# Optimization experiments

Measured on AMD Instinct MI355X. Metric: run time of the kernel, lower is better.

## Reference

```python
import jax, jax.numpy as jnp
import numpy as np

NHID = 512
T_K, T_Q, B = 256, 128, 8


def setup_inputs() -> dict:
    key = jax.random.key(0)
    k1, k2, k3, k4, k5 = jax.random.split(key, 5)
    query = jax.random.normal(k1, (T_Q, B, NHID), dtype=jnp.float32)
    c_key = jax.random.normal(k2, (T_K, B, NHID), dtype=jnp.float32)
    mask = jax.random.randint(k3, (T_K, B), 0, 2).astype(bool)
    # att_mlp params: Linear(2*nhid, nhid) -> Tanh -> Linear(nhid, 1)
    # stored as [in, out] so y = x @ W + b (torch Linear weight transposed)
    W1 = jax.random.normal(k4, (2 * NHID, NHID), dtype=jnp.float32) / np.sqrt(2 * NHID)
    b1 = jnp.zeros((NHID,), dtype=jnp.float32)
    W2 = jax.random.normal(k5, (NHID, 1), dtype=jnp.float32) / np.sqrt(NHID)
    b2 = jnp.zeros((1,), dtype=jnp.float32)
    return {"query": query, "c_key": c_key, "mask": mask,
            "W1": W1, "b1": b1, "W2": W2, "b2": b2}


def reference(query, c_key, mask, W1, b1, W2, b2):
    H = query.shape[-1]
    # cat([k_expand, q_expand], -1) @ W1 == k @ W1[:H] + q @ W1[H:]
    # (avoids materializing the [T_k, T_q, B, 2H] concat the torch code builds)
    k_proj = jnp.einsum('kbh,hd->kbd', c_key, W1[:H])   # [T_k, B, H]
    q_proj = jnp.einsum('qbh,hd->qbd', query, W1[H:])   # [T_q, B, H]
    h = jnp.tanh(k_proj[:, None, :, :] + q_proj[None, :, :, :] + b1)  # [T_k, T_q, B, H]
    att_score = jnp.einsum('kqbh,ho->kqb', h, W2) + b2[0]             # [T_k, T_q, B]
    att_score = jnp.where(mask[:, None, :], -jnp.inf, att_score)
    att_prob = jax.nn.softmax(att_score, axis=0)                      # softmax over keys
    # c_val defaults to c_key in the original forward
    ant_vec = jnp.einsum('kqb,kbh->qbh', att_prob, c_key)             # [T_q, B, H]
    return ant_vec, att_prob
```

## Files before the change

### kernel.cpp

```cpp
#include <hip/hip_runtime.h>
#include <math.h>

#define NHID 512
#define T_K  256
#define T_Q  128
#define BB   8

constexpr float C2L2E = 2.8853900817779268f;
constexpr float L2E   = 1.4426950408889634f;

__device__ __forceinline__ float fexp2(float x) { return __builtin_amdgcn_exp2f(x); }
__device__ __forceinline__ float frcp(float x)  { return __builtin_amdgcn_rcpf(x); }

typedef __attribute__((ext_vector_type(8))) short bf16x8;
typedef __attribute__((ext_vector_type(4))) float f32x4;

__device__ __forceinline__ unsigned short f2bf(float x) {
    unsigned u = __builtin_bit_cast(unsigned, x);
    unsigned r = (u + 0x7FFFu + ((u >> 16) & 1u)) >> 16;
    return (unsigned short)r;
}
__device__ __forceinline__ float bf2f(unsigned short h) {
    unsigned u = ((unsigned)h) << 16;
    return __builtin_bit_cast(float, u);
}

__global__ __launch_bounds__(256) void convert_w1_kernel(
    const float* __restrict__ W1,
    unsigned short* __restrict__ bt_hi, unsigned short* __restrict__ bt_lo)
{
    const int tb = blockIdx.x;
    const int kt = tb & 15;
    const int nt = tb >> 4;
    __shared__ float tile[64][65];
    const int t  = threadIdx.x;
    const int r  = t >> 2;
    const int c0 = (t & 3) * 16;
    const float* src = W1 + (size_t)(kt * 64 + r) * 512 + nt * 64 + c0;
    #pragma unroll
    for (int j = 0; j < 4; ++j) {
        const float4 v = *(const float4*)&src[j * 4];
        tile[r][c0 + j * 4 + 0] = v.x; tile[r][c0 + j * 4 + 1] = v.y;
        tile[r][c0 + j * 4 + 2] = v.z; tile[r][c0 + j * 4 + 3] = v.w;
    }
    __syncthreads();
    const size_t dst = (size_t)((kt >> 3) * 512 + nt * 64 + r) * 512
                     + (size_t)((kt & 7) * 64 + c0);
    #pragma unroll
    for (int j4 = 0; j4 < 4; ++j4) {
        ushort4 h, l;
        #pragma unroll
        for (int e = 0; e < 4; ++e) {
            const float x = tile[c0 + j4 * 4 + e][r];
            const unsigned short hb = f2bf(x);
            ((unsigned short*)&h)[e] = hb;
            ((unsigned short*)&l)[e] = f2bf(x - bf2f(hb));
        }
        *(ushort4*)&bt_hi[dst + j4 * 4] = h;
        *(ushort4*)&bt_lo[dst + j4 * 4] = l;
    }
}

__global__ __launch_bounds__(256) void proj_kernel(
    const float* __restrict__ qry, const float* __restrict__ ckey,
    const unsigned short* __restrict__ bt_hi, const unsigned short* __restrict__ bt_lo,
    const float* __restrict__ b1,
    float* __restrict__ ek, float* __restrict__ eq)
{
    const int row0 = blockIdx.x * 64;
    const int col0 = blockIdx.y * 64;
    const bool isK = row0 < 2048;
    const int bhalf = isK ? 0 : 512;

    __shared__ __align__(16) unsigned short As_h[64 * 64];
    __shared__ __align__(16) unsigned short As_l[64 * 64];
    __shared__ __align__(16) unsigned short Bs_h[64 * 64];
    __shared__ __align__(16) unsigned short Bs_l[64 * 64];

    const int t    = threadIdx.x;
    const int wave = t >> 6;
    const int lane = t & 63;
    const int wm = (wave & 1) * 32;
    const int wn = (wave >> 1) * 32;

    f32x4 acc[2][2] = {};

    const int sr = t >> 2;
    const int sc = (t & 3) * 16;
    const float* gA = (isK ? ckey + (size_t)(row0 + sr) * 512
                           : qry  + (size_t)(row0 - 2048 + sr) * 512) + sc;
    const unsigned short* gBh = bt_hi + (size_t)(bhalf + col0 + sr) * 512 + sc;
    const unsigned short* gBl = bt_lo + (size_t)(bhalf + col0 + sr) * 512 + sc;
    const int c0c = sc >> 3;
    const int sw0 = ((c0c + 0) ^ (sr & 7)) * 8;
    const int sw1 = ((c0c + 1) ^ (sr & 7)) * 8;

    const int quad = lane >> 4, fr = lane & 15;

    for (int k0 = 0; k0 < 512; k0 += 64) {
        __syncthreads();
        {
            float fa[16];
            *(float4*)&fa[0]  = *(const float4*)&gA[k0 + 0];
            *(float4*)&fa[4]  = *(const float4*)&gA[k0 + 4];
            *(float4*)&fa[8]  = *(const float4*)&gA[k0 + 8];
            *(float4*)&fa[12] = *(const float4*)&gA[k0 + 12];
            union { uint4 v; unsigned short s[8]; } h0, l0, h1, l1;
            #pragma unroll
            for (int e = 0; e < 8; ++e) {
                const unsigned short hb = f2bf(fa[e]);
                h0.s[e] = hb; l0.s[e] = f2bf(fa[e] - bf2f(hb));
            }
            #pragma unroll
            for (int e = 0; e < 8; ++e) {
                const unsigned short hb = f2bf(fa[8 + e]);
                h1.s[e] = hb; l1.s[e] = f2bf(fa[8 + e] - bf2f(hb));
            }
            *(uint4*)&As_h[sr * 64 + sw0] = h0.v; *(uint4*)&As_h[sr * 64 + sw1] = h1.v;
            *(uint4*)&As_l[sr * 64 + sw0] = l0.v; *(uint4*)&As_l[sr * 64 + sw1] = l1.v;
            uint4 v0, v1;
            v0 = *(const uint4*)&gBh[k0];     v1 = *(const uint4*)&gBh[k0 + 8];
            *(uint4*)&Bs_h[sr * 64 + sw0] = v0; *(uint4*)&Bs_h[sr * 64 + sw1] = v1;
            v0 = *(const uint4*)&gBl[k0];     v1 = *(const uint4*)&gBl[k0 + 8];
            *(uint4*)&Bs_l[sr * 64 + sw0] = v0; *(uint4*)&Bs_l[sr * 64 + sw1] = v1;
        }
        __syncthreads();
        #pragma unroll
        for (int ks = 0; ks < 2; ++ks) {
            const int cchunk = ks * 4 + quad;
            bf16x8 afh[2], afl[2], bfh[2], bfl[2];
            #pragma unroll
            for (int mt = 0; mt < 2; ++mt) {
                const int m = wm + mt * 16 + fr;
                afh[mt] = *(const bf16x8*)&As_h[m * 64 + ((cchunk ^ (m & 7)) * 8)];
                afl[mt] = *(const bf16x8*)&As_l[m * 64 + ((cchunk ^ (m & 7)) * 8)];
            }
            #pragma unroll
            for (int nt = 0; nt < 2; ++nt) {
                const int n = wn + nt * 16 + fr;
                bfh[nt] = *(const bf16x8*)&Bs_h[n * 64 + ((cchunk ^ (n & 7)) * 8)];
                bfl[nt] = *(const bf16x8*)&Bs_l[n * 64 + ((cchunk ^ (n & 7)) * 8)];
            }
            #pragma unroll
            for (int mt = 0; mt < 2; ++mt)
                #pragma unroll
                for (int nt = 0; nt < 2; ++nt) {
                    acc[mt][nt] = __builtin_amdgcn_mfma_f32_16x16x32_bf16(afh[mt], bfh[nt], acc[mt][nt], 0, 0, 0);
                    acc[mt][nt] = __builtin_amdgcn_mfma_f32_16x16x32_bf16(afh[mt], bfl[nt], acc[mt][nt], 0, 0, 0);
                    acc[mt][nt] = __builtin_amdgcn_mfma_f32_16x16x32_bf16(afl[mt], bfh[nt], acc[mt][nt], 0, 0, 0);
                }
        }
    }

    #pragma unroll
    for (int nt = 0; nt < 2; ++nt) {
        const int colg = col0 + wn + nt * 16 + fr;
        const float b1v = b1[colg];
        #pragma unroll
        for (int mt = 0; mt < 2; ++mt) {
            #pragma unroll
            for (int i = 0; i < 4; ++i) {
                const int rowg = row0 + wm + mt * 16 + quad * 4 + i;
                const float v = acc[mt][nt][i];
                if (isK) ek[(size_t)rowg * 512 + colg] = fexp2((v + b1v) * C2L2E);
                else     eq[(size_t)(rowg - 2048) * 512 + colg] = fexp2(v * C2L2E);
            }
        }
    }
}

__global__ __launch_bounds__(256) void scoreav_kernel(
    const float* __restrict__ ek, const float* __restrict__ eq,
    const float* __restrict__ W2, const float* __restrict__ b2,
    const int* __restrict__ mask, const float* __restrict__ ckey,
    float* __restrict__ prob_out, float* __restrict__ out_ant)
{
    const int t    = threadIdx.x;
    const int lane = t & 63;
    const int wave = __builtin_amdgcn_readfirstlane(t >> 6);
    const int q0   = blockIdx.x * 2;
    const int b    = blockIdx.y;
    const int myk  = wave * 64 + lane;

    __shared__ float eks[2][256 * 19];
    __shared__ float ps[2][256];
    __shared__ float pacc[4][2][512];

    const float4 wA = *(const float4*)&W2[lane * 4];
    const float4 wB = *(const float4*)&W2[256 + lane * 4];
    float s2 = wA.x + wA.y + wA.z + wA.w + wB.x + wB.y + wB.z + wB.w;
    #pragma unroll
    for (int m = 32; m; m >>= 1) s2 += __shfl_xor(s2, m, 64);
    const float base = s2 + b2[0];

    const float* __restrict__ eqr0 = eq + (size_t)(q0 * 8 + b) * 512;
    const float* __restrict__ eqr1 = eq + (size_t)((q0 + 1) * 8 + b) * 512;

    const float* __restrict__ ekg = ek + ((size_t)t * 8 + b) * 512;

    {
        float fa[16];
        *(float4*)&fa[0]  = *(const float4*)&ekg[0];
        *(float4*)&fa[4]  = *(const float4*)&ekg[4];
        *(float4*)&fa[8]  = *(const float4*)&ekg[8];
        *(float4*)&fa[12] = *(const float4*)&ekg[12];
        #pragma unroll
        for (int j = 0; j < 16; ++j) eks[0][t * 19 + j] = fa[j];
    }
    __syncthreads();

    float racc0 = 0.0f, racc1 = 0.0f;

    for (int chunk = 0; chunk < 32; ++chunk) {
        const int buf = chunk & 1;
        const int hc  = chunk * 16;
        float nf[16];
        if (chunk < 31) {
            *(float4*)&nf[0]  = *(const float4*)&ekg[hc + 16];
            *(float4*)&nf[4]  = *(const float4*)&ekg[hc + 20];
            *(float4*)&nf[8]  = *(const float4*)&ekg[hc + 24];
            *(float4*)&nf[12] = *(const float4*)&ekg[hc + 28];
        }
        #pragma unroll
        for (int s = 0; s < 8; ++s) {
            const float ek0 = eks[buf][myk * 19 + 2 * s + 0];
            const float ek1 = eks[buf][myk * 19 + 2 * s + 1];
            const int h = hc + 2 * s;
            const float w0 = W2[h], w1 = W2[h + 1];
            const float e0 = eqr0[h], e1 = eqr0[h + 1];
            const float f0 = eqr1[h], f1 = eqr1[h + 1];
            {
                const float t0 = ek0 * e0, t1 = ek1 * e1;
                const float a0 = t0 + 1.0f, a1 = t1 + 1.0f;
                const float den = a0 * a1;
                const float num = fmaf(w0, a1, w1 * a0);
                racc0 = fmaf(num, frcp(den), racc0);
            }
            {
                const float t0 = ek0 * f0, t1 = ek1 * f1;
                const float a0 = t0 + 1.0f, a1 = t1 + 1.0f;
                const float den = a0 * a1;
                const float num = fmaf(w0, a1, w1 * a0);
                racc1 = fmaf(num, frcp(den), racc1);
            }
        }
        __syncthreads();
        if (chunk < 31) {
            const int nb = buf ^ 1;
            #pragma unroll
            for (int j = 0; j < 16; ++j) eks[nb][t * 19 + j] = nf[j];
        }
        __syncthreads();
    }

    {
        const int msk = mask[myk * 8 + b];
        float s0 = base - 2.0f * racc0;
        float s1 = base - 2.0f * racc1;
        if (msk) { s0 = -INFINITY; s1 = -INFINITY; }
        ps[0][myk] = s0;
        ps[1][myk] = s1;
    }
    __syncthreads();

    if (wave < 2) {
        float4 sv = *(const float4*)&ps[wave][lane * 4];
        float m = fmaxf(fmaxf(sv.x, sv.y), fmaxf(sv.z, sv.w));
        #pragma unroll
        for (int d = 32; d; d >>= 1) m = fmaxf(m, __shfl_xor(m, d, 64));
        float4 pv;
        pv.x = fexp2((sv.x - m) * L2E);
        pv.y = fexp2((sv.y - m) * L2E);
        pv.z = fexp2((sv.z - m) * L2E);
        pv.w = fexp2((sv.w - m) * L2E);
        float sum = pv.x + pv.y + pv.z + pv.w;
        #pragma unroll
        for (int d = 32; d; d >>= 1) sum += __shfl_xor(sum, d, 64);
        const float inv = frcp(sum);
        pv.x *= inv; pv.y *= inv; pv.z *= inv; pv.w *= inv;
        *(float4*)&ps[wave][lane * 4] = pv;
        const int qb_idx = (q0 + wave) * 8 + b;
        const int kbase = lane * 4;
        prob_out[(size_t)(kbase + 0) * 1024 + qb_idx] = pv.x;
        prob_out[(size_t)(kbase + 1) * 1024 + qb_idx] = pv.y;
        prob_out[(size_t)(kbase + 2) * 1024 + qb_idx] = pv.z;
        prob_out[(size_t)(kbase + 3) * 1024 + qb_idx] = pv.w;
    }
    __syncthreads();

    {
        const int h0 = lane * 8;
        float4 aL0 = {}, aH0 = {}, aL1 = {}, aH1 = {};
        const int kstart = wave * 64;
        #pragma unroll 4
        for (int ki = 0; ki < 64; ++ki) {
            const int k = kstart + ki;
            const float* ckp = &ckey[((size_t)k * 8 + b) * 512 + h0];
            const float4 c0 = *(const float4*)&ckp[0];
            const float4 c1 = *(const float4*)&ckp[4];
            const float p0 = ps[0][k];
            const float p1 = ps[1][k];
            aL0.x = fmaf(p0, c0.x, aL0.x); aL0.y = fmaf(p0, c0.y, aL0.y);
            aL0.z = fmaf(p0, c0.z, aL0.z); aL0.w = fmaf(p0, c0.w, aL0.w);
            aH0.x = fmaf(p0, c1.x, aH0.x); aH0.y = fmaf(p0, c1.y, aH0.y);
            aH0.z = fmaf(p0, c1.z, aH0.z); aH0.w = fmaf(p0, c1.w, aH0.w);
            aL1.x = fmaf(p1, c0.x, aL1.x); aL1.y = fmaf(p1, c0.y, aL1.y);
            aL1.z = fmaf(p1, c0.z, aL1.z); aL1.w = fmaf(p1, c0.w, aL1.w);
            aH1.x = fmaf(p1, c1.x, aH1.x); aH1.y = fmaf(p1, c1.y, aH1.y);
            aH1.z = fmaf(p1, c1.z, aH1.z); aH1.w = fmaf(p1, c1.w, aH1.w);
        }
        *(float4*)&pacc[wave][0][h0 + 0] = aL0;
        *(float4*)&pacc[wave][0][h0 + 4] = aH0;
        *(float4*)&pacc[wave][1][h0 + 0] = aL1;
        *(float4*)&pacc[wave][1][h0 + 4] = aH1;
    }
    __syncthreads();

    {
        const int h2 = t * 2;
        #pragma unroll
        for (int qi = 0; qi < 2; ++qi) {
            float2 r0 = *(const float2*)&pacc[0][qi][h2];
            float2 r1 = *(const float2*)&pacc[1][qi][h2];
            float2 r2 = *(const float2*)&pacc[2][qi][h2];
            float2 r3 = *(const float2*)&pacc[3][qi][h2];
            float2 r;
            r.x = (r0.x + r1.x) + (r2.x + r3.x);
            r.y = (r0.y + r1.y) + (r2.y + r3.y);
            *(float2*)&out_ant[((size_t)(q0 + qi) * 8 + b) * 512 + h2] = r;
        }
    }
}

extern "C" void kernel_launch(void* const* d_in, const int* in_sizes, int n_in,
                              void* d_out, int out_size, void* d_ws, size_t ws_size,
                              hipStream_t stream)
{
    const float* qry  = (const float*)d_in[0];
    const float* ckey = (const float*)d_in[1];
    const int*   mask = (const int*)d_in[2];
    const float* W1   = (const float*)d_in[3];
    const float* b1   = (const float*)d_in[4];
    const float* W2   = (const float*)d_in[5];
    const float* b2   = (const float*)d_in[6];

    float* out_ant  = (float*)d_out;
    float* out_prob = (float*)d_out + T_Q * BB * NHID;

    float* ws = (float*)d_ws;
    float* ws_ek = ws;
    float* ws_eq = ws + 1048576;
    unsigned short* bt_hi = (unsigned short*)(ws + 1572864);
    unsigned short* bt_lo = (unsigned short*)(ws + 1835008);

    convert_w1_kernel<<<dim3(128), 256, 0, stream>>>(W1, bt_hi, bt_lo);
    proj_kernel<<<dim3(48, 8), 256, 0, stream>>>(qry, ckey, bt_hi, bt_lo, b1, ws_ek, ws_eq);
    scoreav_kernel<<<dim3(64, 8), 256, 0, stream>>>(ws_ek, ws_eq, W2, b2, mask, ckey,
                                                    out_prob, out_ant);
}
```

Baseline: 126.3 us.

## Transpose exp(k_proj) to [b][h][k] and stream it directly in score kernel

The projection kernel now writes the key-side exponentials in a transposed [batch][hidden][key] layout, so each score thread reads coalesced global loads for its key without LDS staging. The query rows and W2 are staged once into shared memory, which replaces the per-chunk double-buffered LDS tile and its two barriers per chunk. The projection kernel's stores become strided (stride 256 floats along the key index), which may cost write efficiency. The score loop then relies on L2/global latency hiding through unrolling.

After: 118.6 us. 6.1% less time.

```diff
diff --git a/kernel.cpp b/kernel.cpp
--- a/kernel.cpp
+++ b/kernel.cpp
@@ -65,7 +65,7 @@
     const float* __restrict__ qry, const float* __restrict__ ckey,
     const unsigned short* __restrict__ bt_hi, const unsigned short* __restrict__ bt_lo,
     const float* __restrict__ b1,
-    float* __restrict__ ek, float* __restrict__ eq)
+    float* __restrict__ ekt, float* __restrict__ eq)
 {
     const int row0 = blockIdx.x * 64;
     const int col0 = blockIdx.y * 64;
@@ -162,15 +162,20 @@
             for (int i = 0; i < 4; ++i) {
                 const int rowg = row0 + wm + mt * 16 + quad * 4 + i;
                 const float v = acc[mt][nt][i];
-                if (isK) ek[(size_t)rowg * 512 + colg] = fexp2((v + b1v) * C2L2E);
-                else     eq[(size_t)(rowg - 2048) * 512 + colg] = fexp2(v * C2L2E);
+                if (isK) {
+                    const int kidx = rowg >> 3;
+                    const int bb   = rowg & 7;
+                    ekt[((size_t)bb * 512 + colg) * 256 + kidx] = fexp2((v + b1v) * C2L2E);
+                } else {
+                    eq[(size_t)(rowg - 2048) * 512 + colg] = fexp2(v * C2L2E);
+                }
             }
         }
     }
 }
 
 __global__ __launch_bounds__(256) void scoreav_kernel(
-    const float* __restrict__ ek, const float* __restrict__ eq,
+    const float* __restrict__ ekt, const float* __restrict__ eq,
     const float* __restrict__ W2, const float* __restrict__ b2,
     const int* __restrict__ mask, const float* __restrict__ ckey,
     float* __restrict__ prob_out, float* __restrict__ out_ant)
@@ -180,11 +185,19 @@
     const int wave = __builtin_amdgcn_readfirstlane(t >> 6);
     const int q0   = blockIdx.x * 2;
     const int b    = blockIdx.y;
-    const int myk  = wave * 64 + lane;
-
-    __shared__ float eks[2][256 * 19];
+
+    __shared__ float eq0s[512], eq1s[512], w2s[512];
     __shared__ float ps[2][256];
     __shared__ float pacc[4][2][512];
+
+    {
+        const float2 v0 = *(const float2*)&eq[((size_t)q0 * 8 + b) * 512 + t * 2];
+        const float2 v1 = *(const float2*)&eq[((size_t)(q0 + 1) * 8 + b) * 512 + t * 2];
+        const float2 w  = *(const float2*)&W2[t * 2];
+        *(float2*)&eq0s[t * 2] = v0;
+        *(float2*)&eq1s[t * 2] = v1;
+        *(float2*)&w2s[t * 2]  = w;
+    }
 
     const float4 wA = *(const float4*)&W2[lane * 4];
     const float4 wB = *(const float4*)&W2[256 + lane * 4];
@@ -192,74 +205,40 @@
     #pragma unroll
     for (int m = 32; m; m >>= 1) s2 += __shfl_xor(s2, m, 64);
     const float base = s2 + b2[0];
-
-    const float* __restrict__ eqr0 = eq + (size_t)(q0 * 8 + b) * 512;
-    const float* __restrict__ eqr1 = eq + (size_t)((q0 + 1) * 8 + b) * 512;
-
-    const float* __restrict__ ekg = ek + ((size_t)t * 8 + b) * 512;
+    __syncthreads();
+
+    const float* __restrict__ ekb = ekt + (size_t)b * 512 * 256 + t;
+    float racc0 = 0.0f, racc1 = 0.0f;
+
+    #pragma unroll 8
+    for (int hp = 0; hp < 256; ++hp) {
+        const int h = hp * 2;
+        const float ek0 = ekb[(size_t)h * 256];
+        const float ek1 = ekb[(size_t)(h + 1) * 256];
+        const float w0 = w2s[h], w1 = w2s[h + 1];
+        const float e0 = eq0s[h], e1 = eq0s[h + 1];
+        const float f0 = eq1s[h], f1 = eq1s[h + 1];
+        {
+            const float t0 = ek0 * e0, t1 = ek1 * e1;
+            const float a0 = t0 + 1.0f, a1 = t1 + 1.0f;
+            const float num = fmaf(w0, a1, w1 * a0);
+            racc0 = fmaf(num, frcp(a0 * a1), racc0);
+        }
+        {
+            const float t0 = ek0 * f0, t1 = ek1 * f1;
+            const float a0 = t0 + 1.0f, a1 = t1 + 1.0f;
+            const float num = fmaf(w0, a1, w1 * a0);
+            racc1 = fmaf(num, frcp(a0 * a1), racc1);
+        }
+    }
 
     {
-        float fa[16];
-        *(float4*)&fa[0]  = *(const float4*)&ekg[0];
-        *(float4*)&fa[4]  = *(const float4*)&ekg[4];
-        *(float4*)&fa[8]  = *(const float4*)&ekg[8];
-        *(float4*)&fa[12] = *(const float4*)&ekg[12];
-        #pragma unroll
-        for (int j = 0; j < 16; ++j) eks[0][t * 19 + j] = fa[j];
-    }
-    __syncthreads();
-
-    float racc0 = 0.0f, racc1 = 0.0f;
-
-    for (int chunk = 0; chunk < 32; ++chunk) {
-        const int buf = chunk & 1;
-        const int hc  = chunk * 16;
-        float nf[16];
-        if (chunk < 31) {
-            *(float4*)&nf[0]  = *(const float4*)&ekg[hc + 16];
-            *(float4*)&nf[4]  = *(const float4*)&ekg[hc + 20];
-            *(float4*)&nf[8]  = *(const float4*)&ekg[hc + 24];
-            *(float4*)&nf[12] = *(const float4*)&ekg[hc + 28];
-        }
-        #pragma unroll
-        for (int s = 0; s < 8; ++s) {
-            const float ek0 = eks[buf][myk * 19 + 2 * s + 0];
-            const float ek1 = eks[buf][myk * 19 + 2 * s + 1];
-            const int h = hc + 2 * s;
-            const float w0 = W2[h], w1 = W2[h + 1];
-            const float e0 = eqr0[h], e1 = eqr0[h + 1];
-            const float f0 = eqr1[h], f1 = eqr1[h + 1];
-            {
-                const float t0 = ek0 * e0, t1 = ek1 * e1;
-                const float a0 = t0 + 1.0f, a1 = t1 + 1.0f;
-                const float den = a0 * a1;
-                const float num = fmaf(w0, a1, w1 * a0);
-                racc0 = fmaf(num, frcp(den), racc0);
-            }
-            {
-                const float t0 = ek0 * f0, t1 = ek1 * f1;
-                const float a0 = t0 + 1.0f, a1 = t1 + 1.0f;
-                const float den = a0 * a1;
-                const float num = fmaf(w0, a1, w1 * a0);
-                racc1 = fmaf(num, frcp(den), racc1);
-            }
-        }
-        __syncthreads();
-        if (chunk < 31) {
-            const int nb = buf ^ 1;
-            #pragma unroll
-            for (int j = 0; j < 16; ++j) eks[nb][t * 19 + j] = nf[j];
-        }
-        __syncthreads();
-    }
-
-    {
-        const int msk = mask[myk * 8 + b];
+        const int msk = mask[t * 8 + b];
         float s0 = base - 2.0f * racc0;
         float s1 = base - 2.0f * racc1;
         if (msk) { s0 = -INFINITY; s1 = -INFINITY; }
-        ps[0][myk] = s0;
-        ps[1][myk] = s1;
+        ps[0][t] = s0;
+        ps[1][t] = s1;
     }
     __syncthreads();
 
@@ -348,13 +327,13 @@
     float* out_prob = (float*)d_out + T_Q * BB * NHID;
 
     float* ws = (float*)d_ws;
-    float* ws_ek = ws;
-    float* ws_eq = ws + 1048576;
+    float* ws_ekt = ws;
+    float* ws_eq  = ws + 1048576;
     unsigned short* bt_hi = (unsigned short*)(ws + 1572864);
     unsigned short* bt_lo = (unsigned short*)(ws + 1835008);
 
     convert_w1_kernel<<<dim3(128), 256, 0, stream>>>(W1, bt_hi, bt_lo);
-    proj_kernel<<<dim3(48, 8), 256, 0, stream>>>(qry, ckey, bt_hi, bt_lo, b1, ws_ek, ws_eq);
-    scoreav_kernel<<<dim3(64, 8), 256, 0, stream>>>(ws_ek, ws_eq, W2, b2, mask, ckey,
+    proj_kernel<<<dim3(48, 8), 256, 0, stream>>>(qry, ckey, bt_hi, bt_lo, b1, ws_ekt, ws_eq);
+    scoreav_kernel<<<dim3(64, 8), 256, 0, stream>>>(ws_ekt, ws_eq, W2, b2, mask, ckey,
                                                     out_prob, out_ant);
 }
```
